# Optimization experiments

Hardware: AMD Instinct MI355X
Metric: run time of the kernel (lower is better)

Reference implementation:

```python
import jax, jax.numpy as jnp
import numpy as np

D_MODEL, N_HEADS, D_HEAD = 512, 8, 64
NUM_BITS, C_TABLES, PHI_SCALE, MAX_EXP, EPS = 8, 2, 0.1, 4, 1e-6
B, T = 2, 1024


def setup_inputs() -> dict:
    key = jax.random.key(0)
    ks = jax.random.split(key, 7)
    x = jax.random.normal(ks[0], (B, T, D_MODEL), dtype=jnp.float32)
    w_std = 0.02
    Wq = jax.random.normal(ks[1], (D_MODEL, D_MODEL), dtype=jnp.float32) * w_std
    Wk = jax.random.normal(ks[2], (D_MODEL, D_MODEL), dtype=jnp.float32) * w_std
    Wv = jax.random.normal(ks[3], (D_MODEL, D_MODEL), dtype=jnp.float32) * w_std
    Wo = jax.random.normal(ks[4], (D_MODEL, D_MODEL), dtype=jnp.float32) * w_std
    bo = jnp.zeros((D_MODEL,), dtype=jnp.float32)
    # 'positive' init: strictly positive lookup values so phi acts as a kernel feature map
    phi_table = jax.random.uniform(ks[5], (C_TABLES, 2 ** NUM_BITS), dtype=jnp.float32) * 0.5 + 0.01
    return {"x": x, "Wq": Wq, "Wk": Wk, "Wv": Wv, "Wo": Wo, "bo": bo, "phi_table": phi_table}


def _ternary_weight(W):
    # quantize to {-1,0,1} * power-of-two scale (exponent clipped to +/- MAX_EXP), STE-style
    alpha = jnp.mean(jnp.abs(W)) + 1e-12
    e = jnp.clip(jnp.round(jnp.log2(alpha)), -MAX_EXP, MAX_EXP)
    s = jnp.exp2(e)
    Wt = jnp.clip(jnp.round(W / s), -1.0, 1.0) * s
    return W + jax.lax.stop_gradient(Wt - W)


def _ternary_linear(x, W, b=None):
    y = jnp.einsum('btd,ed->bte', x, _ternary_weight(W))
    return y if b is None else y + b


def _phi(x, table):
    # structured lookup activation: sum of c sub-tables indexed at dyadically scaled quantizations
    L = table.shape[1]
    off = L // 2
    y = jnp.zeros_like(x)
    for j in range(table.shape[0]):
        idx = jnp.clip(jnp.round(x / (PHI_SCALE * (2.0 ** j))).astype(jnp.int32) + off, 0, L - 1)
        y = y + table[j][idx]
    return x + jax.lax.stop_gradient(y - x)  # STE: forward = lookup, backward = identity


def reference(x, Wq, Wk, Wv, Wo, bo, phi_table):
    Bsz, Tn, _ = x.shape
    Q = _ternary_linear(x, Wq)
    K = _ternary_linear(x, Wk)
    V = _ternary_linear(x, Wv)

    def split_heads(t):
        return t.reshape(Bsz, Tn, N_HEADS, D_HEAD).transpose(0, 2, 1, 3)  # (B,H,T,d)

    Q, K, V = split_heads(Q), split_heads(K), split_heads(V)
    phiQ = _phi(Q, phi_table)
    phiK = _phi(K, phi_table)

    # causal linear attention via cumulative outer products (faithful to original)
    kv = jnp.einsum('bhnd,bhne->bhnde', phiK, V)            # (B,H,T,d,d)
    kv_cum = jnp.cumsum(kv, axis=2)
    out = jnp.einsum('bhnd,bhnde->bhne', phiQ, kv_cum)       # (B,H,T,d)
    k_cum = jnp.cumsum(phiK, axis=2)
    Z = jnp.clip(jnp.sum(phiQ * k_cum, axis=-1, keepdims=True), EPS, None)
    out = out / Z

    out = out.transpose(0, 2, 1, 3).reshape(Bsz, Tn, D_MODEL)
    return _ternary_linear(out, Wo, bo)
```

## Files before the change

kernel.cpp:

```cpp
#include <hip/hip_runtime.h>
#include <stdint.h>

typedef __bf16 bf16;
typedef __bf16 v8bf __attribute__((ext_vector_type(8)));
typedef float v4f __attribute__((ext_vector_type(4)));

#define T_SEQ   1024
#define D_MODEL 512
#define N_HEADS 8
#define D_HEAD  64
#define B_SZ    2
#define BH      (B_SZ * N_HEADS)
#define CHUNK   128
#define NCHUNK  (T_SEQ / CHUNK)
#define WN      (D_MODEL * D_MODEL)

__device__ __forceinline__ void lds16(const void* g, void* l) {
    __builtin_amdgcn_global_load_lds(
        (const __attribute__((address_space(1))) uint32_t*)g,
        (__attribute__((address_space(3))) uint32_t*)l, 16, 0, 0);
}

struct PreArgs { const float* w[4]; float* partial; const float* x; bf16* xb; };

__global__ __launch_bounds__(256) void k_pre(PreArgs a) {
    const int bid = blockIdx.x, tid = threadIdx.x;
    if (bid < 256) {
        const int mid = bid >> 6, blk = bid & 63;
        const float* __restrict__ W = a.w[mid];
        float sabs = 0.f;
        #pragma unroll
        for (int k = 0; k < 4; ++k) {
            float4 v = ((const float4*)W)[blk * 1024 + k * 256 + tid];
            sabs += fabsf(v.x) + fabsf(v.y) + fabsf(v.z) + fabsf(v.w);
        }
        __shared__ float red[256];
        red[tid] = sabs;
        __syncthreads();
        for (int s = 128; s > 0; s >>= 1) {
            if (tid < s) red[tid] += red[tid + s];
            __syncthreads();
        }
        if (tid == 0) a.partial[mid * 64 + blk] = red[0];
    } else {
        const int i = (bid - 256) * 256 + tid;
        float4 v = ((const float4*)a.x)[i];
        union { uint2 u; bf16 h[4]; } H;
        H.h[0] = (bf16)v.x; H.h[1] = (bf16)v.y;
        H.h[2] = (bf16)v.z; H.h[3] = (bf16)v.w;
        ((uint2*)a.xb)[i] = H.u;
    }
}

struct WqArgs { const float* w[4]; bf16* wt[4]; const float* partial; };

__global__ __launch_bounds__(256) void k_wquant(WqArgs a) {
    const int mid = blockIdx.y, blk = blockIdx.x, tid = threadIdx.x;
    const float* __restrict__ W = a.w[mid];
    bf16* __restrict__ Wt = a.wt[mid];
    __shared__ float sv;
    if (tid < 64) {
        float p = a.partial[mid * 64 + tid];
        #pragma unroll
        for (int w = 1; w < 64; w <<= 1) p += __shfl_xor(p, w);
        if (tid == 0) {
            float alpha = p / (float)WN + 1e-12f;
            float e = rintf(log2f(alpha));
            e = fminf(4.f, fmaxf(-4.f, e));
            sv = exp2f(e);
        }
    }
    __syncthreads();
    const float s = sv;
    const float inv_s = 1.f / s;
    #pragma unroll
    for (int k = 0; k < 4; ++k) {
        const int idx = blk * 1024 + k * 256 + tid;
        float4 v = ((const float4*)W)[idx];
        float vv[4] = {v.x, v.y, v.z, v.w};
        union { uint2 u; bf16 h[4]; } o;
        #pragma unroll
        for (int j = 0; j < 4; ++j) {
            float r = rintf(vv[j] * inv_s);
            r = fminf(1.f, fmaxf(-1.f, r));
            o.h[j] = (bf16)(r * s);
        }
        ((uint2*)Wt)[idx] = o.u;
    }
}

__device__ __forceinline__ void gemm64(
        const char* __restrict__ Ab, const char* __restrict__ Bb,
        bf16* As, bf16* Bs, v4f acc[4]) {
    const int tid = threadIdx.x;
    const int wm = tid >> 6, lane = tid & 63;
    const int q = lane >> 4, r = lane & 15;
    const int lrow = lane >> 3;
    const int schunk = (lane & 7) ^ lrow;
    const int r7 = r & 7;

    for (int k0 = 0; k0 < 512; k0 += 64) {
        #pragma unroll
        for (int j = 0; j < 2; ++j) {
            const int seg = wm * 2 + j;
            const int row = seg * 8 + lrow;
            const size_t goff = (size_t)row * 1024 + (size_t)k0 * 2 + schunk * 16;
            lds16(Ab + goff, (char*)As + (seg << 10));
            lds16(Bb + goff, (char*)Bs + (seg << 10));
        }
        __syncthreads();
        #pragma unroll
        for (int s = 0; s < 2; ++s) {
            const int co = ((s * 4 + q) ^ r7) * 8;
            v8bf ah = *(const v8bf*)&As[(wm * 16 + r) * 64 + co];
            v8bf bb[4];
            #pragma unroll
            for (int v = 0; v < 4; ++v)
                bb[v] = *(const v8bf*)&Bs[(v * 16 + r) * 64 + co];
            #pragma unroll
            for (int v = 0; v < 4; ++v)
                acc[v] = __builtin_amdgcn_mfma_f32_16x16x32_bf16(ah, bb[v], acc[v], 0, 0, 0);
        }
        __syncthreads();
    }
}

struct Qkv2Args {
    const bf16* xb; const bf16* wstk;
    const float* table;
    bf16* phiqB; bf16* phikB; bf16* vbufT;
};

__global__ __launch_bounds__(256) void k_qkv2(Qkv2Args a) {
    __shared__ bf16 As[64 * 64] __attribute__((aligned(16)));
    __shared__ bf16 Bs[64 * 64] __attribute__((aligned(16)));
    __shared__ float tab[512];
    const int tid = threadIdx.x;
    const int tm = blockIdx.x, tn = blockIdx.y;
    const int z = tn >> 3;
    if (z < 2) { tab[tid] = a.table[tid]; tab[tid + 256] = a.table[tid + 256]; }

    v4f acc[4];
    #pragma unroll
    for (int v = 0; v < 4; ++v) acc[v] = (v4f){0.f, 0.f, 0.f, 0.f};

    gemm64((const char*)(a.xb + (size_t)(tm * 64) * 512),
           (const char*)(a.wstk + (size_t)(tn * 64) * 512), As, Bs, acc);

    const int wm = tid >> 6, lane = tid & 63;
    const int q = lane >> 4, r = lane & 15;
    const int h = tn & 7;
    const int mb = tm * 64;
    const int b = mb >> 10, tpos0 = mb & 1023;
    const int bh = b * 8 + h;

    if (z < 2) {
        #pragma unroll
        for (int v = 0; v < 4; ++v) {
            const int d = v * 16 + r;
            #pragma unroll
            for (int i = 0; i < 4; ++i) {
                float val = acc[v][i];
                int i0 = (int)rintf(val / 0.1f) + 128;
                i0 = min(255, max(0, i0));
                int i1 = (int)rintf(val / 0.2f) + 128;
                i1 = min(255, max(0, i1));
                val = tab[i0] + tab[256 + i1];
                As[(wm * 16 + q * 4 + i) * 64 + d] = (bf16)val;
            }
        }
        __syncthreads();
        bf16* dst = (z == 0) ? a.phiqB : a.phikB;
        #pragma unroll
        for (int k = 0; k < 2; ++k) {
            const int idx = k * 256 + tid;
            const int row = idx >> 3, cb = (idx & 7) * 8;
            *(uint4*)&dst[((size_t)bh * 1024 + tpos0 + row) * 64 + cb] =
                *(const uint4*)&As[row * 64 + cb];
        }
    } else {
        const int tpos = tpos0 + wm * 16 + q * 4;
        #pragma unroll
        for (int v = 0; v < 4; ++v) {
            const int d = v * 16 + r;
            union { uint2 pu; bf16 h4[4]; } P;
            #pragma unroll
            for (int i = 0; i < 4; ++i) P.h4[i] = (bf16)acc[v][i];
            *(uint2*)&a.vbufT[((size_t)bh * 64 + d) * 1024 + tpos] = P.pu;
        }
    }
}

__global__ __launch_bounds__(256) void k_chunksum(
        const bf16* __restrict__ phikB, const bf16* __restrict__ vbufT,
        float* __restrict__ kvT, float* __restrict__ ks) {
    const int c = blockIdx.x, bh = blockIdx.y;
    __shared__ float pkF[32 * 64] __attribute__((aligned(16)));
    const int tid = threadIdx.x;
    const int e = tid & 63, g = tid >> 6;
    float kv[16];
    #pragma unroll
    for (int i = 0; i < 16; ++i) kv[i] = 0.f;
    float ksum = 0.f;
    const size_t base = (size_t)bh * 1024 + c * 128;
    const bf16* vrow = vbufT + ((size_t)bh * 64 + e) * 1024 + c * 128;

    for (int sub = 0; sub < 4; ++sub) {
        __syncthreads();
        {
            const int t = tid >> 3, db = (tid & 7) * 8;
            v8bf p = *(const v8bf*)&phikB[(base + sub * 32 + t) * 64 + db];
            #pragma unroll
            for (int j = 0; j < 8; ++j) pkF[t * 64 + db + j] = (float)p[j];
        }
        __syncthreads();
        #pragma unroll
        for (int jv = 0; jv < 4; ++jv) {
            v8bf vch = *(const v8bf*)&vrow[sub * 32 + jv * 8];
            #pragma unroll
            for (int jj = 0; jj < 8; ++jj) {
                const float vv = (float)vch[jj];
                const float4* prow = (const float4*)&pkF[(jv * 8 + jj) * 64 + g * 16];
                float4 p0 = prow[0], p1 = prow[1], p2 = prow[2], p3 = prow[3];
                kv[0]  += p0.x * vv; kv[1]  += p0.y * vv; kv[2]  += p0.z * vv; kv[3]  += p0.w * vv;
                kv[4]  += p1.x * vv; kv[5]  += p1.y * vv; kv[6]  += p1.z * vv; kv[7]  += p1.w * vv;
                kv[8]  += p2.x * vv; kv[9]  += p2.y * vv; kv[10] += p2.z * vv; kv[11] += p2.w * vv;
                kv[12] += p3.x * vv; kv[13] += p3.y * vv; kv[14] += p3.z * vv; kv[15] += p3.w * vv;
            }
        }
        if (tid < 64) {
            #pragma unroll
            for (int t = 0; t < 32; ++t) ksum += pkF[t * 64 + tid];
        }
    }
    const size_t ob = ((size_t)bh * 8 + c) * 4096;
    #pragma unroll
    for (int w4 = 0; w4 < 4; ++w4) {
        float4 s4 = {kv[4 * w4], kv[4 * w4 + 1], kv[4 * w4 + 2], kv[4 * w4 + 3]};
        *(float4*)&kvT[ob + e * 64 + g * 16 + 4 * w4] = s4;
    }
    if (tid < 64) ks[((size_t)bh * 8 + c) * 64 + tid] = ksum;
}

__global__ __launch_bounds__(256) void k_attn(
        const bf16* __restrict__ phiqB, const bf16* __restrict__ phikB,
        const bf16* __restrict__ vbufT, const float* __restrict__ kvT,
        const float* __restrict__ ks, bf16* __restrict__ attn) {
    const int ntile = blockIdx.x, c = blockIdx.y, bh = blockIdx.z;
    __shared__ char smem[56064] __attribute__((aligned(16)));
    bf16* pqs  = (bf16*)smem;
    bf16* kv0s = (bf16*)(smem + 9216);
    bf16* Pbs  = (bf16*)smem;
    bf16* pks  = (bf16*)(smem + 18432);
    bf16* vts  = (bf16*)(smem + 36864);
    float* kc0s = (float*)(smem + 54272);
    float* Zrow = (float*)(smem + 54528);
    float* Zp   = (float*)(smem + 54784);
    float* Zs   = (float*)(smem + 55808);

    const int tid = threadIdx.x;
    const int wid = tid >> 6, lane = tid & 63;
    const int q = lane >> 4, r = lane & 15;
    const size_t tbase = (size_t)bh * 1024 + c * 128;
    const int t0 = ntile * 64;

    #pragma unroll
    for (int k = 0; k < 2; ++k) {
        const int idx = k * 256 + tid;
        const int row = idx >> 3, col = (idx & 7) * 8;
        *(uint4*)&pqs[row * 72 + col] =
            *(const uint4*)&phiqB[(tbase + t0 + row) * 64 + col];
    }
    {
        const int e = tid >> 2, db = (tid & 3) * 16;
        float accp[16];
        #pragma unroll
        for (int j = 0; j < 16; ++j) accp[j] = 0.f;
        for (int cc = 0; cc < c; ++cc) {
            const float* src = kvT + ((size_t)bh * 8 + cc) * 4096 + e * 64 + db;
            #pragma unroll
            for (int k4 = 0; k4 < 4; ++k4) {
                float4 f = *(const float4*)(src + 4 * k4);
                accp[4 * k4]     += f.x; accp[4 * k4 + 1] += f.y;
                accp[4 * k4 + 2] += f.z; accp[4 * k4 + 3] += f.w;
            }
        }
        union { uint4 u; bf16 h8[8]; } U0, U1;
        #pragma unroll
        for (int j = 0; j < 8; ++j) {
            U0.h8[j] = (bf16)accp[j];
            U1.h8[j] = (bf16)accp[8 + j];
        }
        *(uint4*)&kv0s[e * 72 + db] = U0.u;
        *(uint4*)&kv0s[e * 72 + db + 8] = U1.u;
    }
    #pragma unroll
    for (int k = 0; k < 4; ++k) {
        const int idx = k * 256 + tid;
        const int row = idx >> 3, col = (idx & 7) * 8;
        *(uint4*)&pks[row * 72 + col] =
            *(const uint4*)&phikB[(tbase + row) * 64 + col];
        const int row2 = idx >> 4, col2 = (idx & 15) * 8;
        *(uint4*)&vts[row2 * 136 + col2] =
            *(const uint4*)&vbufT[((size_t)bh * 64 + row2) * 1024 + c * 128 + col2];
    }
    if (tid < 64) {
        float s = 0.f;
        for (int cc = 0; cc < c; ++cc) s += ks[((size_t)bh * 8 + cc) * 64 + tid];
        kc0s[tid] = s;
    }
    __syncthreads();

    v4f oacc[4], sacc[8];
    #pragma unroll
    for (int t = 0; t < 4; ++t) oacc[t] = (v4f){0.f, 0.f, 0.f, 0.f};
    #pragma unroll
    for (int u = 0; u < 8; ++u) sacc[u] = (v4f){0.f, 0.f, 0.f, 0.f};
    const int nmt = (ntile == 0) ? 4 : 8;

    #pragma unroll
    for (int kk = 0; kk < 2; ++kk) {
        v8bf af = *(const v8bf*)&pqs[(wid * 16 + r) * 72 + kk * 32 + q * 8];
        #pragma unroll
        for (int t = 0; t < 4; ++t) {
            v8bf bfr = *(const v8bf*)&kv0s[(t * 16 + r) * 72 + kk * 32 + q * 8];
            oacc[t] = __builtin_amdgcn_mfma_f32_16x16x32_bf16(af, bfr, oacc[t], 0, 0, 0);
        }
        #pragma unroll
        for (int u = 0; u < 8; ++u) {
            if (u < nmt) {
                v8bf bk = *(const v8bf*)&pks[(u * 16 + r) * 72 + kk * 32 + q * 8];
                sacc[u] = __builtin_amdgcn_mfma_f32_16x16x32_bf16(af, bk, sacc[u], 0, 0, 0);
            }
        }
    }
    {
        float z0 = 0.f;
        #pragma unroll
        for (int j = 0; j < 16; ++j)
            z0 += (float)pqs[lane * 72 + wid * 16 + j] * kc0s[wid * 16 + j];
        Zp[wid * 64 + lane] = z0;
    }
    __syncthreads();

    float zi[4] = {0.f, 0.f, 0.f, 0.f};
    #pragma unroll
    for (int u = 0; u < 8; ++u) {
        if (u < nmt) {
            const int m = u * 16 + r;
            #pragma unroll
            for (int i = 0; i < 4; ++i) {
                const int nloc = t0 + wid * 16 + q * 4 + i;
                const float sv = (m <= nloc) ? sacc[u][i] : 0.f;
                zi[i] += sv;
                Pbs[(wid * 16 + q * 4 + i) * 136 + m] = (bf16)sv;
            }
        }
    }
    #pragma unroll
    for (int w = 1; w < 16; w <<= 1) {
        #pragma unroll
        for (int i = 0; i < 4; ++i) zi[i] += __shfl_xor(zi[i], w);
    }
    if (r == 0) {
        #pragma unroll
        for (int i = 0; i < 4; ++i) Zrow[wid * 16 + q * 4 + i] = zi[i];
    }
    __syncthreads();

    if (tid < 64)
        Zs[tid] = fmaxf(Zrow[tid] + Zp[tid] + Zp[64 + tid] + Zp[128 + tid] + Zp[192 + tid],
                        1e-6f);
    __syncthreads();

    const int nkk = (ntile == 0) ? 2 : 4;
    #pragma unroll
    for (int kk = 0; kk < 4; ++kk) {
        if (kk < nkk) {
            v8bf af = *(const v8bf*)&Pbs[(wid * 16 + r) * 136 + kk * 32 + q * 8];
            #pragma unroll
            for (int t = 0; t < 4; ++t) {
                v8bf bfr = *(const v8bf*)&vts[(t * 16 + r) * 136 + kk * 32 + q * 8];
                oacc[t] = __builtin_amdgcn_mfma_f32_16x16x32_bf16(af, bfr, oacc[t], 0, 0, 0);
            }
        }
    }

    const int b = bh >> 3, h = bh & 7;
    #pragma unroll
    for (int t = 0; t < 4; ++t) {
        const int e = t * 16 + r;
        #pragma unroll
        for (int i = 0; i < 4; ++i) {
            const int row = wid * 16 + q * 4 + i;
            const float val = oacc[t][i] / Zs[row];
            const size_t mtok = (size_t)b * 1024 + c * 128 + t0 + row;
            attn[mtok * 512 + h * 64 + e] = (bf16)val;
        }
    }
}

struct OArgs { const bf16* attn; const bf16* wo; const float* bo; float* y; };

__global__ __launch_bounds__(256) void k_oproj(OArgs a) {
    __shared__ bf16 As[64 * 64] __attribute__((aligned(16)));
    __shared__ bf16 Bs[64 * 64] __attribute__((aligned(16)));
    v4f acc[4];
    #pragma unroll
    for (int v = 0; v < 4; ++v) acc[v] = (v4f){0.f, 0.f, 0.f, 0.f};
    gemm64((const char*)(a.attn + (size_t)(blockIdx.x * 64) * 512),
           (const char*)(a.wo + (size_t)(blockIdx.y * 64) * 512), As, Bs, acc);

    const int tid = threadIdx.x;
    const int wm = tid >> 6, lane = tid & 63;
    const int q = lane >> 4, r = lane & 15;
    #pragma unroll
    for (int v = 0; v < 4; ++v) {
        const int n = blockIdx.y * 64 + v * 16 + r;
        const float bias = a.bo[n];
        #pragma unroll
        for (int i = 0; i < 4; ++i) {
            const int m = blockIdx.x * 64 + wm * 16 + q * 4 + i;
            a.y[(size_t)m * 512 + n] = acc[v][i] + bias;
        }
    }
}

extern "C" void kernel_launch(void* const* d_in, const int* in_sizes, int n_in,
                              void* d_out, int out_size, void* d_ws, size_t ws_size,
                              hipStream_t stream) {
    const float* x   = (const float*)d_in[0];
    const float* Wq  = (const float*)d_in[1];
    const float* Wk  = (const float*)d_in[2];
    const float* Wv  = (const float*)d_in[3];
    const float* Wo  = (const float*)d_in[4];
    const float* bo  = (const float*)d_in[5];
    const float* tab = (const float*)d_in[6];

    uint8_t* w = (uint8_t*)d_ws;
    bf16* wt     = (bf16*)w;
    bf16* xb     = wt + 4 * WN;
    bf16* phiqB  = xb + 1048576;
    bf16* phikB  = phiqB + (size_t)16 * 1024 * 64;
    bf16* vbufT  = phikB + (size_t)16 * 1024 * 64;
    float* kvT   = (float*)(vbufT + (size_t)16 * 64 * 1024);
    float* ks    = kvT + (size_t)16 * 8 * 4096;
    bf16* attn   = (bf16*)(ks + 16 * 8 * 64);
    float* partial = (float*)(attn + (size_t)2048 * 512);

    PreArgs pr;
    pr.w[0] = Wq; pr.w[1] = Wk; pr.w[2] = Wv; pr.w[3] = Wo;
    pr.partial = partial; pr.x = x; pr.xb = xb;
    k_pre<<<dim3(1280), dim3(256), 0, stream>>>(pr);

    WqArgs qa;
    qa.w[0] = Wq; qa.w[1] = Wk; qa.w[2] = Wv; qa.w[3] = Wo;
    qa.wt[0] = wt; qa.wt[1] = wt + WN; qa.wt[2] = wt + 2 * WN; qa.wt[3] = wt + 3 * WN;
    qa.partial = partial;
    k_wquant<<<dim3(64, 4), dim3(256), 0, stream>>>(qa);

    Qkv2Args pa{ xb, wt, tab, phiqB, phikB, vbufT };
    k_qkv2<<<dim3(32, 24), dim3(256), 0, stream>>>(pa);

    k_chunksum<<<dim3(NCHUNK, BH), dim3(256), 0, stream>>>(phikB, vbufT, kvT, ks);
    k_attn<<<dim3(2, NCHUNK, BH), dim3(256), 0, stream>>>(phiqB, phikB, vbufT, kvT, ks, attn);

    OArgs oa{ attn, wt + 3 * WN, bo, (float*)d_out };
    k_oproj<<<dim3(32, 8), dim3(256), 0, stream>>>(oa);
}
```

Measured before the change: 124.5 us.

## Fuse chunk KV-state summation into attention kernel via MFMA over prior chunks

Removes the separate chunk-sum kernel and its fp32 kv/ks intermediates. The qkv kernel now also writes a transposed phiK buffer, and each attention block recomputes the prefix KV state directly with bf16 MFMA over all preceding chunks, plus the running phiK sum. This saves a kernel launch and the fp32 round-trip through memory, but adds redundant work: both ntile blocks of a chunk recompute the prefix, and later chunks do up to seven chunks of matmul, which unbalances the load.

```diff
diff --git a/kernel.cpp b/kernel.cpp
--- a/kernel.cpp
+++ b/kernel.cpp
@@ -128,7 +128,7 @@
 struct Qkv2Args {
     const bf16* xb; const bf16* wstk;
     const float* table;
-    bf16* phiqB; bf16* phikB; bf16* vbufT;
+    bf16* phiqB; bf16* phikB; bf16* phikT; bf16* vbufT;
 };
 
 __global__ __launch_bounds__(256) void k_qkv2(Qkv2Args a) {
@@ -153,11 +153,13 @@
     const int mb = tm * 64;
     const int b = mb >> 10, tpos0 = mb & 1023;
     const int bh = b * 8 + h;
+    const int tpos = tpos0 + wm * 16 + q * 4;
 
     if (z < 2) {
         #pragma unroll
         for (int v = 0; v < 4; ++v) {
             const int d = v * 16 + r;
+            union { uint2 pu; bf16 h4[4]; } P;
             #pragma unroll
             for (int i = 0; i < 4; ++i) {
                 float val = acc[v][i];
@@ -167,7 +169,10 @@
                 i1 = min(255, max(0, i1));
                 val = tab[i0] + tab[256 + i1];
                 As[(wm * 16 + q * 4 + i) * 64 + d] = (bf16)val;
+                P.h4[i] = (bf16)val;
             }
+            if (z == 1)
+                *(uint2*)&a.phikT[((size_t)bh * 64 + d) * 1024 + tpos] = P.pu;
         }
         __syncthreads();
         bf16* dst = (z == 0) ? a.phiqB : a.phikB;
@@ -179,7 +184,6 @@
                 *(const uint4*)&As[row * 64 + cb];
         }
     } else {
-        const int tpos = tpos0 + wm * 16 + q * 4;
         #pragma unroll
         for (int v = 0; v < 4; ++v) {
             const int d = v * 16 + r;
@@ -191,61 +195,10 @@
     }
 }
 
-__global__ __launch_bounds__(256) void k_chunksum(
-        const bf16* __restrict__ phikB, const bf16* __restrict__ vbufT,
-        float* __restrict__ kvT, float* __restrict__ ks) {
-    const int c = blockIdx.x, bh = blockIdx.y;
-    __shared__ float pkF[32 * 64] __attribute__((aligned(16)));
-    const int tid = threadIdx.x;
-    const int e = tid & 63, g = tid >> 6;
-    float kv[16];
-    #pragma unroll
-    for (int i = 0; i < 16; ++i) kv[i] = 0.f;
-    float ksum = 0.f;
-    const size_t base = (size_t)bh * 1024 + c * 128;
-    const bf16* vrow = vbufT + ((size_t)bh * 64 + e) * 1024 + c * 128;
-
-    for (int sub = 0; sub < 4; ++sub) {
-        __syncthreads();
-        {
-            const int t = tid >> 3, db = (tid & 7) * 8;
-            v8bf p = *(const v8bf*)&phikB[(base + sub * 32 + t) * 64 + db];
-            #pragma unroll
-            for (int j = 0; j < 8; ++j) pkF[t * 64 + db + j] = (float)p[j];
-        }
-        __syncthreads();
-        #pragma unroll
-        for (int jv = 0; jv < 4; ++jv) {
-            v8bf vch = *(const v8bf*)&vrow[sub * 32 + jv * 8];
-            #pragma unroll
-            for (int jj = 0; jj < 8; ++jj) {
-                const float vv = (float)vch[jj];
-                const float4* prow = (const float4*)&pkF[(jv * 8 + jj) * 64 + g * 16];
-                float4 p0 = prow[0], p1 = prow[1], p2 = prow[2], p3 = prow[3];
-                kv[0]  += p0.x * vv; kv[1]  += p0.y * vv; kv[2]  += p0.z * vv; kv[3]  += p0.w * vv;
-                kv[4]  += p1.x * vv; kv[5]  += p1.y * vv; kv[6]  += p1.z * vv; kv[7]  += p1.w * vv;
-                kv[8]  += p2.x * vv; kv[9]  += p2.y * vv; kv[10] += p2.z * vv; kv[11] += p2.w * vv;
-                kv[12] += p3.x * vv; kv[13] += p3.y * vv; kv[14] += p3.z * vv; kv[15] += p3.w * vv;
-            }
-        }
-        if (tid < 64) {
-            #pragma unroll
-            for (int t = 0; t < 32; ++t) ksum += pkF[t * 64 + tid];
-        }
-    }
-    const size_t ob = ((size_t)bh * 8 + c) * 4096;
-    #pragma unroll
-    for (int w4 = 0; w4 < 4; ++w4) {
-        float4 s4 = {kv[4 * w4], kv[4 * w4 + 1], kv[4 * w4 + 2], kv[4 * w4 + 3]};
-        *(float4*)&kvT[ob + e * 64 + g * 16 + 4 * w4] = s4;
-    }
-    if (tid < 64) ks[((size_t)bh * 8 + c) * 64 + tid] = ksum;
-}
-
 __global__ __launch_bounds__(256) void k_attn(
         const bf16* __restrict__ phiqB, const bf16* __restrict__ phikB,
-        const bf16* __restrict__ vbufT, const float* __restrict__ kvT,
-        const float* __restrict__ ks, bf16* __restrict__ attn) {
+        const bf16* __restrict__ phikT, const bf16* __restrict__ vbufT,
+        bf16* __restrict__ attn) {
     const int ntile = blockIdx.x, c = blockIdx.y, bh = blockIdx.z;
     __shared__ char smem[56064] __attribute__((aligned(16)));
     bf16* pqs  = (bf16*)smem;
@@ -253,6 +206,8 @@
     bf16* Pbs  = (bf16*)smem;
     bf16* pks  = (bf16*)(smem + 18432);
     bf16* vts  = (bf16*)(smem + 36864);
+    bf16* tB   = (bf16*)(smem + 18432);
+    bf16* tA   = (bf16*)(smem + 36864);
     float* kc0s = (float*)(smem + 54272);
     float* Zrow = (float*)(smem + 54528);
     float* Zp   = (float*)(smem + 54784);
@@ -271,29 +226,47 @@
         *(uint4*)&pqs[row * 72 + col] =
             *(const uint4*)&phiqB[(tbase + t0 + row) * 64 + col];
     }
-    {
-        const int e = tid >> 2, db = (tid & 3) * 16;
-        float accp[16];
-        #pragma unroll
-        for (int j = 0; j < 16; ++j) accp[j] = 0.f;
-        for (int cc = 0; cc < c; ++cc) {
-            const float* src = kvT + ((size_t)bh * 8 + cc) * 4096 + e * 64 + db;
-            #pragma unroll
-            for (int k4 = 0; k4 < 4; ++k4) {
-                float4 f = *(const float4*)(src + 4 * k4);
-                accp[4 * k4]     += f.x; accp[4 * k4 + 1] += f.y;
-                accp[4 * k4 + 2] += f.z; accp[4 * k4 + 3] += f.w;
+
+    v4f kvacc[4];
+    #pragma unroll
+    for (int v = 0; v < 4; ++v) kvacc[v] = (v4f){0.f, 0.f, 0.f, 0.f};
+    float kcp = 0.f;
+    const int srow = tid >> 2, scol = (tid & 3) * 32;
+    const int kd = tid & 63, ktq = tid >> 6;
+    for (int cc = 0; cc < c; ++cc) {
+        __syncthreads();
+        #pragma unroll
+        for (int j = 0; j < 4; ++j) {
+            *(uint4*)&tB[srow * 136 + scol + j * 8] =
+                *(const uint4*)&phikT[((size_t)bh * 64 + srow) * 1024 + cc * 128 + scol + j * 8];
+            *(uint4*)&tA[srow * 136 + scol + j * 8] =
+                *(const uint4*)&vbufT[((size_t)bh * 64 + srow) * 1024 + cc * 128 + scol + j * 8];
+        }
+        __syncthreads();
+        #pragma unroll
+        for (int kk = 0; kk < 4; ++kk) {
+            v8bf av = *(const v8bf*)&tA[(wid * 16 + r) * 136 + kk * 32 + q * 8];
+            #pragma unroll
+            for (int v = 0; v < 4; ++v) {
+                v8bf bd = *(const v8bf*)&tB[(v * 16 + r) * 136 + kk * 32 + q * 8];
+                kvacc[v] = __builtin_amdgcn_mfma_f32_16x16x32_bf16(av, bd, kvacc[v], 0, 0, 0);
             }
         }
-        union { uint4 u; bf16 h8[8]; } U0, U1;
-        #pragma unroll
-        for (int j = 0; j < 8; ++j) {
-            U0.h8[j] = (bf16)accp[j];
-            U1.h8[j] = (bf16)accp[8 + j];
-        }
-        *(uint4*)&kv0s[e * 72 + db] = U0.u;
-        *(uint4*)&kv0s[e * 72 + db + 8] = U1.u;
-    }
+        #pragma unroll
+        for (int j4 = 0; j4 < 4; ++j4) {
+            v8bf p = *(const v8bf*)&tB[kd * 136 + ktq * 32 + j4 * 8];
+            #pragma unroll
+            for (int jj = 0; jj < 8; ++jj) kcp += (float)p[jj];
+        }
+    }
+    #pragma unroll
+    for (int v = 0; v < 4; ++v)
+        #pragma unroll
+        for (int i = 0; i < 4; ++i)
+            kv0s[(wid * 16 + q * 4 + i) * 72 + v * 16 + r] = (bf16)kvacc[v][i];
+    Zp[ktq * 64 + kd] = kcp;
+    __syncthreads();
+
     #pragma unroll
     for (int k = 0; k < 4; ++k) {
         const int idx = k * 256 + tid;
@@ -304,11 +277,8 @@
         *(uint4*)&vts[row2 * 136 + col2] =
             *(const uint4*)&vbufT[((size_t)bh * 64 + row2) * 1024 + c * 128 + col2];
     }
-    if (tid < 64) {
-        float s = 0.f;
-        for (int cc = 0; cc < c; ++cc) s += ks[((size_t)bh * 8 + cc) * 64 + tid];
-        kc0s[tid] = s;
-    }
+    if (tid < 64)
+        kc0s[tid] = Zp[tid] + Zp[64 + tid] + Zp[128 + tid] + Zp[192 + tid];
     __syncthreads();
 
     v4f oacc[4], sacc[8];
@@ -442,10 +412,9 @@
     bf16* xb     = wt + 4 * WN;
     bf16* phiqB  = xb + 1048576;
     bf16* phikB  = phiqB + (size_t)16 * 1024 * 64;
-    bf16* vbufT  = phikB + (size_t)16 * 1024 * 64;
-    float* kvT   = (float*)(vbufT + (size_t)16 * 64 * 1024);
-    float* ks    = kvT + (size_t)16 * 8 * 4096;
-    bf16* attn   = (bf16*)(ks + 16 * 8 * 64);
+    bf16* phikT  = phikB + (size_t)16 * 1024 * 64;
+    bf16* vbufT  = phikT + (size_t)16 * 64 * 1024;
+    bf16* attn   = vbufT + (size_t)16 * 64 * 1024;
     float* partial = (float*)(attn + (size_t)2048 * 512);
 
     PreArgs pr;
@@ -459,11 +428,10 @@
     qa.partial = partial;
     k_wquant<<<dim3(64, 4), dim3(256), 0, stream>>>(qa);
 
-    Qkv2Args pa{ xb, wt, tab, phiqB, phikB, vbufT };
+    Qkv2Args pa{ xb, wt, tab, phiqB, phikB, phikT, vbufT };
     k_qkv2<<<dim3(32, 24), dim3(256), 0, stream>>>(pa);
 
-    k_chunksum<<<dim3(NCHUNK, BH), dim3(256), 0, stream>>>(phikB, vbufT, kvT, ks);
-    k_attn<<<dim3(2, NCHUNK, BH), dim3(256), 0, stream>>>(phiqB, phikB, vbufT, kvT, ks, attn);
+    k_attn<<<dim3(2, NCHUNK, BH), dim3(256), 0, stream>>>(phiqB, phikB, phikT, vbufT, attn);
 
     OArgs oa{ attn, wt + 3 * WN, bo, (float*)d_out };
     k_oproj<<<dim3(32, 8), dim3(256), 0, stream>>>(oa);
```

New measurement: 106.4 us. 14.6% less time.
